# Kernel optimization log

Hardware: AMD Instinct MI355X
Metric: run time of the kernel (lower is better)

The kernel has to match this reference:

```python
import jax, jax.numpy as jnp
import numpy as np

D_MODEL = 1024
N_HEAD = 16
SEQ = 2048
BATCH = 2


def setup_inputs() -> dict:
    key = jax.random.key(0)
    x = jax.random.normal(key, (BATCH, SEQ, D_MODEL), dtype=jnp.float32)
    return {"x": x}


def reference(x) -> jnp.ndarray:
    B, S, D = x.shape
    H = N_HEAD
    hd = D // H
    # split heads: q=k=v=x -> [B, H, S, hd]
    qkv = x.reshape(B, S, H, hd).transpose(0, 2, 1, 3)
    q = k = v = qkv
    # scores [B, H, S, S], scaled by sqrt(head_dim)
    w = jnp.einsum("bhqd,bhkd->bhqk", q, k) / jnp.sqrt(jnp.asarray(hd, x.dtype))
    # causal mask (nd == ns == S here)
    causal = jnp.tril(jnp.ones((S, S), dtype=bool))
    mask_value = jnp.finfo(w.dtype).min
    w = jnp.where(causal[None, None, :, :], w, mask_value)
    w = jax.nn.softmax(w, axis=-1)
    out = jnp.einsum("bhqk,bhkd->bhqd", w, v)
    # merge heads -> [B, S, D]
    return out.transpose(0, 2, 1, 3).reshape(B, S, D)
```

## Files before the change

### kernel.cpp

```cpp
#include <hip/hip_runtime.h>

#define BATCH  2
#define SEQ    2048
#define DMODEL 1024
#define NHEAD  16
#define HD     64
#define BH     (BATCH * NHEAD)

typedef __attribute__((ext_vector_type(8))) short s8v;
typedef __attribute__((ext_vector_type(4))) float f4v;

__device__ inline unsigned short bf16_rne(float f) {
    unsigned u = __builtin_bit_cast(unsigned, f);
    u += 0x7FFFu + ((u >> 16) & 1u);
    return (unsigned short)(u >> 16);
}

__global__ __launch_bounds__(256) void prep_kernel(const float* __restrict__ x,
                                                   unsigned short* __restrict__ xb,
                                                   unsigned short* __restrict__ xbT) {
    __shared__ unsigned short tile[64 * 66];
    const int id = blockIdx.x;
    const int bh = id & (BH - 1);
    const int st = id >> 5;
    const int b = bh >> 4, h = bh & (NHEAD - 1);
    const int s0 = st * 64;
    const int tid = threadIdx.x;
    const int c4 = tid & 15, r16 = tid >> 4;

#pragma unroll
    for (int p = 0; p < 4; ++p) {
        const int sl = p * 16 + r16;
        const size_t off = (size_t)(b * SEQ + s0 + sl) * DMODEL + h * HD + c4 * 4;
        float4 v = *(const float4*)(x + off);
        ushort4 o;
        o.x = bf16_rne(v.x); o.y = bf16_rne(v.y);
        o.z = bf16_rne(v.z); o.w = bf16_rne(v.w);
        *(ushort4*)(xb + off) = o;
        unsigned short* t = tile + sl * 66 + c4 * 4;
        t[0] = o.x; t[1] = o.y; t[2] = o.z; t[3] = o.w;
    }
    __syncthreads();
#pragma unroll
    for (int p = 0; p < 4; ++p) {
        const int d = p * 16 + r16;
        ushort4 o;
        o.x = tile[(c4 * 4 + 0) * 66 + d];
        o.y = tile[(c4 * 4 + 1) * 66 + d];
        o.z = tile[(c4 * 4 + 2) * 66 + d];
        o.w = tile[(c4 * 4 + 3) * 66 + d];
        *(ushort4*)(xbT + (size_t)(bh * HD + d) * SEQ + s0 + c4 * 4) = o;
    }
}

__global__ __launch_bounds__(256, 2) void flash_kernel(const unsigned short* __restrict__ xb,
                                                       const unsigned short* __restrict__ xbT,
                                                       float* __restrict__ out) {
    __shared__ __align__(16) char lds[24576];

    const int id = blockIdx.x;
    const int bh = id & (BH - 1);
    const int qt = (SEQ / 64 - 1) - (id >> 5);
    const int b = bh >> 4, h = bh & (NHEAD - 1);
    const int tid = threadIdx.x;
    const int w = tid >> 6;
    const int lane = tid & 63;
    const int n = lane & 15;
    const int g = lane >> 4;
    const int qbase = qt * 64;

    const unsigned short* xbh = xb + (size_t)b * SEQ * DMODEL + h * HD;
    const unsigned short* xTh = xbT + (size_t)bh * HD * SEQ;

    const int qrow = qbase + w * 16 + n;
    const s8v qf0 = *(const s8v*)(xbh + (size_t)qrow * DMODEL + g * 8);
    const s8v qf1 = *(const s8v*)(xbh + (size_t)qrow * DMODEL + 32 + g * 8);

    int roff0[4], roff1[4];
#pragma unroll
    for (int t = 0; t < 4; ++t) {
        roff0[t] = (t * 16 + n) * 128 + ((g ^ (n & 7)) * 16);
        roff1[t] = (t * 16 + n) * 128 + (((4 + g) ^ (n & 7)) * 16);
    }

    f4v o0 = {0.f, 0.f, 0.f, 0.f}, o1 = o0, o2 = o0, o3 = o0, l4 = o0;
    char* const Pbase = lds + 16384 + w * 2048;

    const int sr = lane >> 3;
    const int sc = lane & 7;

    for (int kt = 0; kt <= qt; ++kt) {
        const int k0 = kt * 64;
        __syncthreads();
        if (w < 2) {
#pragma unroll
            for (int i = 0; i < 4; ++i) {
                const int r = w * 32 + i * 8 + sr;
                const unsigned short* gsrc =
                    xbh + (size_t)(k0 + r) * DMODEL + ((sc ^ (r & 7)) * 8);
                const int loff = __builtin_amdgcn_readfirstlane((w * 32 + i * 8) * 128);
                __builtin_amdgcn_global_load_lds(
                    (const __attribute__((address_space(1))) void*)gsrc,
                    (__attribute__((address_space(3))) void*)(lds + loff), 16, 0, 0);
            }
        } else {
#pragma unroll
            for (int i = 0; i < 4; ++i) {
                const int d = (w - 2) * 32 + i * 8 + sr;
                const unsigned short* gsrc =
                    xTh + (size_t)d * SEQ + k0 + ((sc ^ (d & 7)) * 8);
                const int loff =
                    __builtin_amdgcn_readfirstlane(8192 + ((w - 2) * 32 + i * 8) * 128);
                __builtin_amdgcn_global_load_lds(
                    (const __attribute__((address_space(1))) void*)gsrc,
                    (__attribute__((address_space(3))) void*)(lds + loff), 16, 0, 0);
            }
        }
        __syncthreads();

        const bool diag = (kt == qt);
#pragma unroll
        for (int t = 0; t < 4; ++t) {
            const s8v kb0 = *(const s8v*)(lds + roff0[t]);
            const s8v kb1 = *(const s8v*)(lds + roff1[t]);
            f4v c = {0.f, 0.f, 0.f, 0.f};
            c = __builtin_amdgcn_mfma_f32_16x16x32_bf16(qf0, kb0, c, 0, 0, 0);
            c = __builtin_amdgcn_mfma_f32_16x16x32_bf16(qf1, kb1, c, 0, 0, 0);
#pragma unroll
            for (int r = 0; r < 4; ++r) {
                float p = __builtin_amdgcn_exp2f(c[r] * 0.18033688011112042f);
                if (diag)
                    p = ((t * 16 + n) <= (w * 16 + g * 4 + r)) ? p : 0.0f;
                l4[r] += p;
                const int Lp = (g * 4 + r) | ((((t * 2) + (n >> 3)) & 3) << 4);
                *(unsigned short*)(Pbase + (t >> 1) * 1024 + Lp * 16 + (n & 7) * 2) =
                    bf16_rne(p);
            }
        }

        const s8v pa0 = *(const s8v*)(Pbase + lane * 16);
        const s8v pa1 = *(const s8v*)(Pbase + 1024 + lane * 16);
        const char* kColB = lds + 8192;
        {
            s8v vb;
            vb = *(const s8v*)(kColB + roff0[0]);
            o0 = __builtin_amdgcn_mfma_f32_16x16x32_bf16(pa0, vb, o0, 0, 0, 0);
            vb = *(const s8v*)(kColB + roff1[0]);
            o0 = __builtin_amdgcn_mfma_f32_16x16x32_bf16(pa1, vb, o0, 0, 0, 0);
            vb = *(const s8v*)(kColB + roff0[1]);
            o1 = __builtin_amdgcn_mfma_f32_16x16x32_bf16(pa0, vb, o1, 0, 0, 0);
            vb = *(const s8v*)(kColB + roff1[1]);
            o1 = __builtin_amdgcn_mfma_f32_16x16x32_bf16(pa1, vb, o1, 0, 0, 0);
            vb = *(const s8v*)(kColB + roff0[2]);
            o2 = __builtin_amdgcn_mfma_f32_16x16x32_bf16(pa0, vb, o2, 0, 0, 0);
            vb = *(const s8v*)(kColB + roff1[2]);
            o2 = __builtin_amdgcn_mfma_f32_16x16x32_bf16(pa1, vb, o2, 0, 0, 0);
            vb = *(const s8v*)(kColB + roff0[3]);
            o3 = __builtin_amdgcn_mfma_f32_16x16x32_bf16(pa0, vb, o3, 0, 0, 0);
            vb = *(const s8v*)(kColB + roff1[3]);
            o3 = __builtin_amdgcn_mfma_f32_16x16x32_bf16(pa1, vb, o3, 0, 0, 0);
        }
    }

#pragma unroll
    for (int m = 1; m < 16; m <<= 1) {
        l4[0] += __shfl_xor(l4[0], m, 64);
        l4[1] += __shfl_xor(l4[1], m, 64);
        l4[2] += __shfl_xor(l4[2], m, 64);
        l4[3] += __shfl_xor(l4[3], m, 64);
    }
    f4v inv;
    inv[0] = 1.0f / l4[0];
    inv[1] = 1.0f / l4[1];
    inv[2] = 1.0f / l4[2];
    inv[3] = 1.0f / l4[3];

    float* outh = out + (size_t)b * SEQ * DMODEL + h * HD;
#pragma unroll
    for (int r = 0; r < 4; ++r) {
        const size_t rowoff = (size_t)(qbase + w * 16 + g * 4 + r) * DMODEL;
        outh[rowoff + 0 * 16 + n] = o0[r] * inv[r];
        outh[rowoff + 1 * 16 + n] = o1[r] * inv[r];
        outh[rowoff + 2 * 16 + n] = o2[r] * inv[r];
        outh[rowoff + 3 * 16 + n] = o3[r] * inv[r];
    }
}

#define KT 32
#define QR 16
#define LDS_STRIDE 68

__global__ __launch_bounds__(64, 2)
void attn_fp32_kernel(const float* __restrict__ x, float* __restrict__ out) {
    __shared__ float kv[KT * LDS_STRIDE];
    const int id = blockIdx.x;
    const int bh = id & (BATCH * NHEAD - 1);
    const int qt = (SEQ / QR - 1) - (id >> 5);
    const int b = bh >> 4, h = bh & (NHEAD - 1);
    const int lane = threadIdx.x;
    const int row = lane & (QR - 1);
    const int slice = lane >> 4;
    const int qrow = qt * QR + row;
    const float* xh = x + (size_t)b * SEQ * DMODEL + (size_t)h * HD;
    float q[HD], o[HD];
    const float4* qp = (const float4*)(xh + (size_t)qrow * DMODEL);
#pragma unroll
    for (int i = 0; i < HD / 4; ++i) {
        float4 v = qp[i];
        q[4*i+0] = v.x * 0.125f; q[4*i+1] = v.y * 0.125f;
        q[4*i+2] = v.z * 0.125f; q[4*i+3] = v.w * 0.125f;
    }
#pragma unroll
    for (int d = 0; d < HD; ++d) o[d] = 0.0f;
    float l = 0.0f;
    const int kend = qt * QR + QR;
    for (int kt0 = 0; kt0 < kend; kt0 += KT) {
        __syncthreads();
#pragma unroll
        for (int i = 0; i < (KT * HD / 4) / 64; ++i) {
            int idx = i * 64 + lane;
            int r = idx >> 4, c = idx & 15;
            *(float4*)(kv + r * LDS_STRIDE + c * 4) =
                *(const float4*)(xh + (size_t)(kt0 + r) * DMODEL + c * 4);
        }
        __syncthreads();
#pragma unroll 2
        for (int jj = 0; jj < KT / 4; ++jj) {
            const int j = jj * 4 + slice;
            const float* kr = kv + j * LDS_STRIDE;
            float a0 = 0.f, a1 = 0.f, a2 = 0.f, a3 = 0.f;
#pragma unroll
            for (int dq = 0; dq < 16; ++dq) {
                float4 kk = ((const float4*)kr)[dq];
                a0 = fmaf(q[4*dq+0], kk.x, a0); a1 = fmaf(q[4*dq+1], kk.y, a1);
                a2 = fmaf(q[4*dq+2], kk.z, a2); a3 = fmaf(q[4*dq+3], kk.w, a3);
            }
            float p = __expf((a0 + a1) + (a2 + a3));
            p = (kt0 + j <= qrow) ? p : 0.0f;
            l += p;
#pragma unroll
            for (int dq = 0; dq < 16; ++dq) {
                float4 vv = ((const float4*)kr)[dq];
                o[4*dq+0] = fmaf(p, vv.x, o[4*dq+0]); o[4*dq+1] = fmaf(p, vv.y, o[4*dq+1]);
                o[4*dq+2] = fmaf(p, vv.z, o[4*dq+2]); o[4*dq+3] = fmaf(p, vv.w, o[4*dq+3]);
            }
        }
    }
    l += __shfl_xor(l, 16, 64);
    l += __shfl_xor(l, 32, 64);
#pragma unroll
    for (int d = 0; d < HD; ++d) {
        o[d] += __shfl_xor(o[d], 16, 64);
        o[d] += __shfl_xor(o[d], 32, 64);
    }
    if (slice == 0) {
        const float invl = 1.0f / l;
        float4* op = (float4*)(out + ((size_t)b * SEQ + qrow) * DMODEL + (size_t)h * HD);
#pragma unroll
        for (int i = 0; i < HD / 4; ++i) {
            float4 v;
            v.x = o[4*i+0] * invl; v.y = o[4*i+1] * invl;
            v.z = o[4*i+2] * invl; v.w = o[4*i+3] * invl;
            op[i] = v;
        }
    }
}

extern "C" void kernel_launch(void* const* d_in, const int* in_sizes, int n_in,
                              void* d_out, int out_size, void* d_ws, size_t ws_size,
                              hipStream_t stream) {
    const float* x = (const float*)d_in[0];
    float* out = (float*)d_out;
    const size_t need = (size_t)2 * BATCH * SEQ * DMODEL * 2;
    if (ws_size >= need) {
        unsigned short* xb  = (unsigned short*)d_ws;
        unsigned short* xbT = xb + (size_t)BATCH * SEQ * DMODEL;
        hipLaunchKernelGGL(prep_kernel, dim3(BH * SEQ / 64), dim3(256), 0, stream, x, xb, xbT);
        hipLaunchKernelGGL(flash_kernel, dim3(BH * SEQ / 64), dim3(256), 0, stream, xb, xbT, out);
    } else {
        hipLaunchKernelGGL(attn_fp32_kernel, dim3(BATCH * NHEAD * (SEQ / QR)), dim3(64), 0,
                           stream, x, out);
    }
}
```

Before: 112.1 us.

## Enlarge flash query tile to 128 rows, keep P in registers via transposed S

The flash kernel now handles 128 query rows per block, each wave covering 32 rows in two 16-row subtiles, so every K/V tile loaded into LDS is reused twice as much. Scores are computed as K·Q^T, which lets the bf16 probabilities be packed directly into the operand layout of the 16x16x16 MFMA for the PV product. This removes the LDS round-trip for P and the P staging buffer. The prep kernel also packs bf16 pairs into 32-bit words for the transpose. In exchange there are half as many blocks, which hurts load balance on the causal triangle, and more registers are live per thread.

```diff
diff --git a/kernel.cpp b/kernel.cpp
--- a/kernel.cpp
+++ b/kernel.cpp
@@ -8,6 +8,7 @@
 #define BH     (BATCH * NHEAD)
 
 typedef __attribute__((ext_vector_type(8))) short s8v;
+typedef __attribute__((ext_vector_type(4))) short s4v;
 typedef __attribute__((ext_vector_type(4))) float f4v;
 
 __device__ inline unsigned short bf16_rne(float f) {
@@ -15,181 +16,189 @@
     u += 0x7FFFu + ((u >> 16) & 1u);
     return (unsigned short)(u >> 16);
 }
-
+__device__ inline unsigned pack_bf16(float lo, float hi) {
+    return (unsigned)bf16_rne(lo) | ((unsigned)bf16_rne(hi) << 16);
+}
+
+#if __has_builtin(__builtin_amdgcn_mfma_f32_16x16x16bf16_1k)
+__device__ inline f4v mfma16(s4v a, s4v b, f4v c) {
+    return __builtin_amdgcn_mfma_f32_16x16x16bf16_1k(a, b, c, 0, 0, 0);
+}
+#else
+__device__ inline f4v mfma16(s4v a, s4v b, f4v c) {
+    f4v d;
+    asm("v_mfma_f32_16x16x16_bf16 %0, %1, %2, %3" : "=v"(d) : "v"(a), "v"(b), "v"(c));
+    return d;
+}
+#endif
+
+#define PSTR 34
 __global__ __launch_bounds__(256) void prep_kernel(const float* __restrict__ x,
                                                    unsigned short* __restrict__ xb,
                                                    unsigned short* __restrict__ xbT) {
-    __shared__ unsigned short tile[64 * 66];
+    __shared__ unsigned tile[64 * PSTR];
     const int id = blockIdx.x;
     const int bh = id & (BH - 1);
     const int st = id >> 5;
     const int b = bh >> 4, h = bh & (NHEAD - 1);
     const int s0 = st * 64;
     const int tid = threadIdx.x;
-    const int c4 = tid & 15, r16 = tid >> 4;
+    const int c4 = tid & 15;
+    const int r16 = tid >> 4;
 
 #pragma unroll
     for (int p = 0; p < 4; ++p) {
         const int sl = p * 16 + r16;
         const size_t off = (size_t)(b * SEQ + s0 + sl) * DMODEL + h * HD + c4 * 4;
         float4 v = *(const float4*)(x + off);
-        ushort4 o;
-        o.x = bf16_rne(v.x); o.y = bf16_rne(v.y);
-        o.z = bf16_rne(v.z); o.w = bf16_rne(v.w);
-        *(ushort4*)(xb + off) = o;
-        unsigned short* t = tile + sl * 66 + c4 * 4;
-        t[0] = o.x; t[1] = o.y; t[2] = o.z; t[3] = o.w;
+        unsigned lo = pack_bf16(v.x, v.y);
+        unsigned hi = pack_bf16(v.z, v.w);
+        *(uint2*)(xb + off) = make_uint2(lo, hi);
+        *(uint2*)(tile + sl * PSTR + c4 * 2) = make_uint2(lo, hi);
     }
     __syncthreads();
-#pragma unroll
-    for (int p = 0; p < 4; ++p) {
-        const int d = p * 16 + r16;
-        ushort4 o;
-        o.x = tile[(c4 * 4 + 0) * 66 + d];
-        o.y = tile[(c4 * 4 + 1) * 66 + d];
-        o.z = tile[(c4 * 4 + 2) * 66 + d];
-        o.w = tile[(c4 * 4 + 3) * 66 + d];
-        *(ushort4*)(xbT + (size_t)(bh * HD + d) * SEQ + s0 + c4 * 4) = o;
+
+#pragma unroll
+    for (int it = 0; it < 2; ++it) {
+        const int dp = it * 16 + r16;
+        unsigned w0 = tile[(c4 * 4 + 0) * PSTR + dp];
+        unsigned w1 = tile[(c4 * 4 + 1) * PSTR + dp];
+        unsigned w2 = tile[(c4 * 4 + 2) * PSTR + dp];
+        unsigned w3 = tile[(c4 * 4 + 3) * PSTR + dp];
+        unsigned lo01 = (w0 & 0xFFFFu) | (w1 << 16);
+        unsigned lo23 = (w2 & 0xFFFFu) | (w3 << 16);
+        unsigned hi01 = (w0 >> 16) | (w1 & 0xFFFF0000u);
+        unsigned hi23 = (w2 >> 16) | (w3 & 0xFFFF0000u);
+        const size_t base = (size_t)(bh * HD + 2 * dp) * SEQ + s0 + c4 * 4;
+        *(uint2*)(xbT + base) = make_uint2(lo01, lo23);
+        *(uint2*)(xbT + base + SEQ) = make_uint2(hi01, hi23);
     }
 }
 
 __global__ __launch_bounds__(256, 2) void flash_kernel(const unsigned short* __restrict__ xb,
                                                        const unsigned short* __restrict__ xbT,
                                                        float* __restrict__ out) {
-    __shared__ __align__(16) char lds[24576];
+    __shared__ __align__(16) char lds[16384];
 
     const int id = blockIdx.x;
     const int bh = id & (BH - 1);
-    const int qt = (SEQ / 64 - 1) - (id >> 5);
+    const int qt = (SEQ / 128 - 1) - (id >> 5);
     const int b = bh >> 4, h = bh & (NHEAD - 1);
     const int tid = threadIdx.x;
     const int w = tid >> 6;
     const int lane = tid & 63;
     const int n = lane & 15;
     const int g = lane >> 4;
-    const int qbase = qt * 64;
+    const int qbase = qt * 128 + w * 32;
 
     const unsigned short* xbh = xb + (size_t)b * SEQ * DMODEL + h * HD;
     const unsigned short* xTh = xbT + (size_t)bh * HD * SEQ;
 
-    const int qrow = qbase + w * 16 + n;
-    const s8v qf0 = *(const s8v*)(xbh + (size_t)qrow * DMODEL + g * 8);
-    const s8v qf1 = *(const s8v*)(xbh + (size_t)qrow * DMODEL + 32 + g * 8);
-
-    int roff0[4], roff1[4];
-#pragma unroll
-    for (int t = 0; t < 4; ++t) {
-        roff0[t] = (t * 16 + n) * 128 + ((g ^ (n & 7)) * 16);
-        roff1[t] = (t * 16 + n) * 128 + (((4 + g) ^ (n & 7)) * 16);
-    }
-
-    f4v o0 = {0.f, 0.f, 0.f, 0.f}, o1 = o0, o2 = o0, o3 = o0, l4 = o0;
-    char* const Pbase = lds + 16384 + w * 2048;
-
-    const int sr = lane >> 3;
-    const int sc = lane & 7;
-
-    for (int kt = 0; kt <= qt; ++kt) {
+    s8v qf[2][2];
+#pragma unroll
+    for (int qs = 0; qs < 2; ++qs)
+#pragma unroll
+        for (int dh = 0; dh < 2; ++dh)
+            qf[qs][dh] = *(const s8v*)(xbh + (size_t)(qbase + qs * 16 + n) * DMODEL +
+                                       dh * 32 + g * 8);
+
+    f4v O[2][4];
+#pragma unroll
+    for (int qs = 0; qs < 2; ++qs)
+#pragma unroll
+        for (int t = 0; t < 4; ++t) O[qs][t] = (f4v){0.f, 0.f, 0.f, 0.f};
+    float l[2] = {0.f, 0.f};
+
+    const int sw = n & 7;
+    int kchunk[2];
+#pragma unroll
+    for (int dh = 0; dh < 2; ++dh) kchunk[dh] = ((dh * 4 + g) ^ sw) * 16;
+    int vchunk[4];
+#pragma unroll
+    for (int tt = 0; tt < 4; ++tt)
+        vchunk[tt] = (((tt * 2 + (g >> 1)) ^ sw) * 16) + (g & 1) * 8;
+
+    const int sr = lane >> 3, sc = lane & 7;
+    const int ktend = 2 * qt + 1;
+
+    for (int kt = 0; kt <= ktend; ++kt) {
         const int k0 = kt * 64;
         __syncthreads();
-        if (w < 2) {
-#pragma unroll
-            for (int i = 0; i < 4; ++i) {
-                const int r = w * 32 + i * 8 + sr;
-                const unsigned short* gsrc =
-                    xbh + (size_t)(k0 + r) * DMODEL + ((sc ^ (r & 7)) * 8);
-                const int loff = __builtin_amdgcn_readfirstlane((w * 32 + i * 8) * 128);
-                __builtin_amdgcn_global_load_lds(
-                    (const __attribute__((address_space(1))) void*)gsrc,
-                    (__attribute__((address_space(3))) void*)(lds + loff), 16, 0, 0);
-            }
-        } else {
-#pragma unroll
-            for (int i = 0; i < 4; ++i) {
-                const int d = (w - 2) * 32 + i * 8 + sr;
-                const unsigned short* gsrc =
-                    xTh + (size_t)d * SEQ + k0 + ((sc ^ (d & 7)) * 8);
-                const int loff =
-                    __builtin_amdgcn_readfirstlane(8192 + ((w - 2) * 32 + i * 8) * 128);
-                __builtin_amdgcn_global_load_lds(
-                    (const __attribute__((address_space(1))) void*)gsrc,
-                    (__attribute__((address_space(3))) void*)(lds + loff), 16, 0, 0);
-            }
-        }
-        __syncthreads();
-
-        const bool diag = (kt == qt);
+#pragma unroll
+        for (int i = 0; i < 2; ++i) {
+            const int r = w * 16 + i * 8 + sr;
+            const int loff = __builtin_amdgcn_readfirstlane((w * 16 + i * 8) * 128);
+            const unsigned short* gK = xbh + (size_t)(k0 + r) * DMODEL + ((sc ^ (r & 7)) * 8);
+            __builtin_amdgcn_global_load_lds(
+                (const __attribute__((address_space(1))) void*)gK,
+                (__attribute__((address_space(3))) void*)(lds + loff), 16, 0, 0);
+            const unsigned short* gV = xTh + (size_t)r * SEQ + k0 + ((sc ^ (r & 7)) * 8);
+            __builtin_amdgcn_global_load_lds(
+                (const __attribute__((address_space(1))) void*)gV,
+                (__attribute__((address_space(3))) void*)(lds + 8192 + loff), 16, 0, 0);
+        }
+        __syncthreads();
+
+        const bool msk = (kt >= 2 * qt);
+        s4v P[2][4];
+#pragma unroll
+        for (int tt = 0; tt < 4; ++tt) {
+            const int rowb = (tt * 16 + n) * 128;
+            const s8v ka0 = *(const s8v*)(lds + rowb + kchunk[0]);
+            const s8v ka1 = *(const s8v*)(lds + rowb + kchunk[1]);
+#pragma unroll
+            for (int qs = 0; qs < 2; ++qs) {
+                f4v c = {0.f, 0.f, 0.f, 0.f};
+                c = __builtin_amdgcn_mfma_f32_16x16x32_bf16(ka0, qf[qs][0], c, 0, 0, 0);
+                c = __builtin_amdgcn_mfma_f32_16x16x32_bf16(ka1, qf[qs][1], c, 0, 0, 0);
+#pragma unroll
+                for (int r = 0; r < 4; ++r) {
+                    float p = __builtin_amdgcn_exp2f(c[r] * 0.18033688011112042f);
+                    if (msk)
+                        p = (k0 + tt * 16 + g * 4 + r <= qbase + qs * 16 + n) ? p : 0.f;
+                    l[qs] += p;
+                    c[r] = p;
+                }
+                unsigned p01 = pack_bf16(c[0], c[1]);
+                unsigned p23 = pack_bf16(c[2], c[3]);
+                P[qs][tt] = __builtin_bit_cast(s4v, make_uint2(p01, p23));
+            }
+        }
 #pragma unroll
         for (int t = 0; t < 4; ++t) {
-            const s8v kb0 = *(const s8v*)(lds + roff0[t]);
-            const s8v kb1 = *(const s8v*)(lds + roff1[t]);
-            f4v c = {0.f, 0.f, 0.f, 0.f};
-            c = __builtin_amdgcn_mfma_f32_16x16x32_bf16(qf0, kb0, c, 0, 0, 0);
-            c = __builtin_amdgcn_mfma_f32_16x16x32_bf16(qf1, kb1, c, 0, 0, 0);
-#pragma unroll
-            for (int r = 0; r < 4; ++r) {
-                float p = __builtin_amdgcn_exp2f(c[r] * 0.18033688011112042f);
-                if (diag)
-                    p = ((t * 16 + n) <= (w * 16 + g * 4 + r)) ? p : 0.0f;
-                l4[r] += p;
-                const int Lp = (g * 4 + r) | ((((t * 2) + (n >> 3)) & 3) << 4);
-                *(unsigned short*)(Pbase + (t >> 1) * 1024 + Lp * 16 + (n & 7) * 2) =
-                    bf16_rne(p);
-            }
-        }
-
-        const s8v pa0 = *(const s8v*)(Pbase + lane * 16);
-        const s8v pa1 = *(const s8v*)(Pbase + 1024 + lane * 16);
-        const char* kColB = lds + 8192;
-        {
-            s8v vb;
-            vb = *(const s8v*)(kColB + roff0[0]);
-            o0 = __builtin_amdgcn_mfma_f32_16x16x32_bf16(pa0, vb, o0, 0, 0, 0);
-            vb = *(const s8v*)(kColB + roff1[0]);
-            o0 = __builtin_amdgcn_mfma_f32_16x16x32_bf16(pa1, vb, o0, 0, 0, 0);
-            vb = *(const s8v*)(kColB + roff0[1]);
-            o1 = __builtin_amdgcn_mfma_f32_16x16x32_bf16(pa0, vb, o1, 0, 0, 0);
-            vb = *(const s8v*)(kColB + roff1[1]);
-            o1 = __builtin_amdgcn_mfma_f32_16x16x32_bf16(pa1, vb, o1, 0, 0, 0);
-            vb = *(const s8v*)(kColB + roff0[2]);
-            o2 = __builtin_amdgcn_mfma_f32_16x16x32_bf16(pa0, vb, o2, 0, 0, 0);
-            vb = *(const s8v*)(kColB + roff1[2]);
-            o2 = __builtin_amdgcn_mfma_f32_16x16x32_bf16(pa1, vb, o2, 0, 0, 0);
-            vb = *(const s8v*)(kColB + roff0[3]);
-            o3 = __builtin_amdgcn_mfma_f32_16x16x32_bf16(pa0, vb, o3, 0, 0, 0);
-            vb = *(const s8v*)(kColB + roff1[3]);
-            o3 = __builtin_amdgcn_mfma_f32_16x16x32_bf16(pa1, vb, o3, 0, 0, 0);
-        }
-    }
-
-#pragma unroll
-    for (int m = 1; m < 16; m <<= 1) {
-        l4[0] += __shfl_xor(l4[0], m, 64);
-        l4[1] += __shfl_xor(l4[1], m, 64);
-        l4[2] += __shfl_xor(l4[2], m, 64);
-        l4[3] += __shfl_xor(l4[3], m, 64);
-    }
-    f4v inv;
-    inv[0] = 1.0f / l4[0];
-    inv[1] = 1.0f / l4[1];
-    inv[2] = 1.0f / l4[2];
-    inv[3] = 1.0f / l4[3];
-
+            const int rowb = 8192 + (t * 16 + n) * 128;
+#pragma unroll
+            for (int tt = 0; tt < 4; ++tt) {
+                const s4v vb = *(const s4v*)(lds + rowb + vchunk[tt]);
+                O[0][t] = mfma16(P[0][tt], vb, O[0][t]);
+                O[1][t] = mfma16(P[1][tt], vb, O[1][t]);
+            }
+        }
+    }
+
+#pragma unroll
+    for (int qs = 0; qs < 2; ++qs) {
+        l[qs] += __shfl_xor(l[qs], 16, 64);
+        l[qs] += __shfl_xor(l[qs], 32, 64);
+    }
     float* outh = out + (size_t)b * SEQ * DMODEL + h * HD;
 #pragma unroll
-    for (int r = 0; r < 4; ++r) {
-        const size_t rowoff = (size_t)(qbase + w * 16 + g * 4 + r) * DMODEL;
-        outh[rowoff + 0 * 16 + n] = o0[r] * inv[r];
-        outh[rowoff + 1 * 16 + n] = o1[r] * inv[r];
-        outh[rowoff + 2 * 16 + n] = o2[r] * inv[r];
-        outh[rowoff + 3 * 16 + n] = o3[r] * inv[r];
+    for (int qs = 0; qs < 2; ++qs) {
+#pragma unroll
+        for (int r = 0; r < 4; ++r) {
+            const float inv = 1.0f / __shfl(l[qs], g * 4 + r, 64);
+            float* op = outh + (size_t)(qbase + qs * 16 + g * 4 + r) * DMODEL + n;
+            op[0]  = O[qs][0][r] * inv;
+            op[16] = O[qs][1][r] * inv;
+            op[32] = O[qs][2][r] * inv;
+            op[48] = O[qs][3][r] * inv;
+        }
     }
 }
 
 #define KT 32
 #define QR 16
 #define LDS_STRIDE 68
-
 __global__ __launch_bounds__(64, 2)
 void attn_fp32_kernel(const float* __restrict__ x, float* __restrict__ out) {
     __shared__ float kv[KT * LDS_STRIDE];
@@ -276,7 +285,7 @@
         unsigned short* xb  = (unsigned short*)d_ws;
         unsigned short* xbT = xb + (size_t)BATCH * SEQ * DMODEL;
         hipLaunchKernelGGL(prep_kernel, dim3(BH * SEQ / 64), dim3(256), 0, stream, x, xb, xbT);
-        hipLaunchKernelGGL(flash_kernel, dim3(BH * SEQ / 64), dim3(256), 0, stream, xb, xbT, out);
+        hipLaunchKernelGGL(flash_kernel, dim3(BH * SEQ / 128), dim3(256), 0, stream, xb, xbT, out);
     } else {
         hipLaunchKernelGGL(attn_fp32_kernel, dim3(BATCH * NHEAD * (SEQ / QR)), dim3(64), 0,
                            stream, x, out);
```

After: 116.8 us. 1.04x slower.
